# Optimization experiments

Measured on AMD Instinct MI355X. Metric: run time of the kernel, lower is better.

## Reference

```python
import jax, jax.numpy as jnp
import numpy as np

NEG = -9e15


def setup_inputs() -> dict:
    key = jax.random.key(0)
    k1, k2, k3, k4, k5 = jax.random.split(key, 5)
    N, D_IN, D_OUT = 8192, 512, 128
    x = jax.random.normal(k1, (N, D_IN), dtype=jnp.float32)
    adj = jax.random.randint(k2, (N, N), 0, 2, dtype=jnp.int32)
    W_fc = jax.random.normal(k3, (D_IN, D_OUT), dtype=jnp.float32) * (1.0 / np.sqrt(D_IN))
    w_a1 = jax.random.normal(k4, (D_OUT,), dtype=jnp.float32) * (1.0 / np.sqrt(D_OUT))
    w_a2 = jax.random.normal(k5, (D_OUT,), dtype=jnp.float32) * (1.0 / np.sqrt(D_OUT))
    return {"x": x, "adj": adj, "W_fc": W_fc, "w_a1": w_a1, "w_a2": w_a2}


def reference(x, adj, W_fc, w_a1, w_a2):
    # h = fc(x): [N, d_out]
    h = x @ W_fc
    # a1, a2: [N] projections; outer-sum scores a1[i] + a2[j] -> [N, N]
    a1 = h @ w_a1
    a2 = h @ w_a2
    scores = a1[:, None] + a2[None, :]
    # adjacency mask + row softmax
    scores = jnp.where(adj > 0, scores, jnp.float32(NEG))
    attention = jax.nn.softmax(scores, axis=-1)
    # weighted aggregation: [N, N] @ [N, d_out]
    out = attention @ h
    return out  # act == 'None', so no relu
```

## Files before the change

### kernel.cpp

```cpp
#include <hip/hip_runtime.h>
#include <hip/hip_bf16.h>


#define NN 8192
#define DIN 512
#define DOUT 128

typedef __attribute__((ext_vector_type(4))) int   int4v;
typedef __attribute__((ext_vector_type(4))) float f32x4;
typedef __attribute__((ext_vector_type(8))) short bf16x8;

static __device__ __forceinline__ unsigned short f2bf(float f) {
    unsigned u = __float_as_uint(f);
    return (unsigned short)((u + 0x7FFFu + ((u >> 16) & 1u)) >> 16);
}
static __device__ __forceinline__ float bf2f(unsigned short b) {
    return __uint_as_float((unsigned)b << 16);
}
static __device__ __forceinline__ void gload_lds16(const void* g, void* l) {
    __builtin_amdgcn_global_load_lds(
        (const __attribute__((address_space(1))) unsigned*)g,
        (__attribute__((address_space(3))) unsigned*)l, 16, 0, 0);
}
static __device__ __forceinline__ int4v ntld(const int* p) {
    return __builtin_nontemporal_load(reinterpret_cast<const int4v*>(p));
}

__global__ __launch_bounds__(256) void k_cvtW(const float* __restrict__ W,
                                              unsigned short* __restrict__ WT) {
    __shared__ float s[8][128];
    const int t  = threadIdx.x;
    const int k0 = blockIdx.x * 8;
    {
        int idx = t * 4;
        int k = idx >> 7, d = idx & 127;
        float4 v = *reinterpret_cast<const float4*>(&W[(size_t)(k0 + k) * DOUT + d]);
        *reinterpret_cast<float4*>(&s[k][d]) = v;
    }
    __syncthreads();
    const int d  = t & 127;
    const int pl = t >> 7;
    unsigned short o[8];
    #pragma unroll
    for (int kk = 0; kk < 8; ++kk) {
        float f = s[kk][d];
        unsigned short hb = f2bf(f);
        o[kk] = pl ? f2bf(f - bf2f(hb)) : hb;
    }
    *reinterpret_cast<uint4*>(&WT[(size_t)pl * 128 * DIN + (size_t)d * DIN + k0]) =
        *reinterpret_cast<const uint4*>(o);
}

__global__ __launch_bounds__(512, 2) void k_h(const float* __restrict__ x,
                                              const unsigned short* __restrict__ WT,
                                              const float* __restrict__ wa2,
                                              unsigned short* __restrict__ Gt) {
    __shared__ __align__(16) char xls[16384];
    __shared__ float red[8][16];
    __shared__ float es[16];
    const int t = threadIdx.x;
    const int w = t >> 6, l = t & 63;
    const int c = l & 15, g = l >> 4;
    const int j0 = blockIdx.x * 16;

    f32x4 acc = (f32x4)0.f;

    const int srow = t >> 5;
    const int sc4  = t & 31;
    const unsigned wbyte = (unsigned)srow * 256 +
                           (((unsigned)(sc4 * 8)) ^ (((unsigned)(srow & 15)) << 4));
    const float* xp = x + (size_t)(j0 + srow) * DIN + sc4 * 4;

    const unsigned short* bhp = WT + (size_t)(w * 16 + c) * DIN + g * 8;
    const unsigned short* blp = bhp + 128 * DIN;
    const unsigned rswz = ((unsigned)c) << 4;

    float4 xv = *reinterpret_cast<const float4*>(xp);

    for (int kt = 0; kt < 4; ++kt) {
        const int cur = kt & 1;
        char* ph = xls + (cur * 2 + 0) * 4096;
        char* pl_ = xls + (cur * 2 + 1) * 4096;
        {
            float vf[4] = {xv.x, xv.y, xv.z, xv.w};
            unsigned short hb[4], lb[4];
            #pragma unroll
            for (int e2 = 0; e2 < 4; ++e2) {
                hb[e2] = f2bf(vf[e2]);
                lb[e2] = f2bf(vf[e2] - bf2f(hb[e2]));
            }
            uint2 hv = {(unsigned)hb[0] | ((unsigned)hb[1] << 16),
                        (unsigned)hb[2] | ((unsigned)hb[3] << 16)};
            uint2 lv = {(unsigned)lb[0] | ((unsigned)lb[1] << 16),
                        (unsigned)lb[2] | ((unsigned)lb[3] << 16)};
            *reinterpret_cast<uint2*>(ph  + wbyte) = hv;
            *reinterpret_cast<uint2*>(pl_ + wbyte) = lv;
        }
        if (kt < 3) xv = *reinterpret_cast<const float4*>(xp + (kt + 1) * 128);
        __syncthreads();
        #pragma unroll
        for (int ks = 0; ks < 4; ++ks) {
            unsigned ro = ((unsigned)(ks * 64 + g * 16)) ^ rswz;
            bf16x8 ah = *reinterpret_cast<const bf16x8*>(ph  + c * 256 + ro);
            bf16x8 al = *reinterpret_cast<const bf16x8*>(pl_ + c * 256 + ro);
            bf16x8 bh = *reinterpret_cast<const bf16x8*>(bhp + kt * 128 + ks * 32);
            bf16x8 bl = *reinterpret_cast<const bf16x8*>(blp + kt * 128 + ks * 32);
            acc = __builtin_amdgcn_mfma_f32_16x16x32_bf16(ah, bh, acc, 0, 0, 0);
            acc = __builtin_amdgcn_mfma_f32_16x16x32_bf16(ah, bl, acc, 0, 0, 0);
            acc = __builtin_amdgcn_mfma_f32_16x16x32_bf16(al, bh, acc, 0, 0, 0);
        }
        __syncthreads();
    }

    const float wl = wa2[w * 16 + c];
    #pragma unroll
    for (int r = 0; r < 4; ++r) {
        float p = acc[r] * wl;
        p += __shfl_xor(p, 1); p += __shfl_xor(p, 2);
        p += __shfl_xor(p, 4); p += __shfl_xor(p, 8);
        if (c == 0) red[w][g * 4 + r] = p;
    }
    __syncthreads();
    if (t < 16) {
        float s = 0.f;
        #pragma unroll
        for (int ww = 0; ww < 8; ++ww) s += red[ww][t];
        es[t] = expf(s);
    }
    __syncthreads();
    {
        unsigned short b[4];
        #pragma unroll
        for (int r = 0; r < 4; ++r) b[r] = f2bf(acc[r] * es[g * 4 + r]);
        uint2 uv = {(unsigned)b[0] | ((unsigned)b[1] << 16),
                    (unsigned)b[2] | ((unsigned)b[3] << 16)};
        *reinterpret_cast<uint2*>(&Gt[(size_t)(w * 16 + c) * NN + j0 + g * 4]) = uv;
    }
    if (t < 8) {
        unsigned u = (unsigned)f2bf(es[t * 2]) | ((unsigned)f2bf(es[t * 2 + 1]) << 16);
        reinterpret_cast<unsigned*>(&Gt[(size_t)128 * NN + j0])[t] = u;
    }
}

__global__ __launch_bounds__(512, 2) void k_gat(const int* __restrict__ adj,
                                                const unsigned short* __restrict__ Gt,
                                                float* __restrict__ out) {
    __shared__ __align__(16) char lds[86144];
    const int t = threadIdx.x;
    const int w = t >> 6, l = t & 63;
    const int c = l & 15, g = l >> 4;
    const int wm = w >> 2, wc = w & 3;
    const int row0 = blockIdx.x * 32;

    float* denp  = (float*)(lds + 81920);
    float* den_l = (float*)(lds + 86016);

    f32x4 acc0 = (f32x4)0.f, acc1 = (f32x4)0.f;

    const int r0 = t >> 5;
    const int kg = t & 31;
    const int* ap0 = adj + (size_t)(row0 + r0) * NN + kg * 4;
    const int* ap1 = adj + (size_t)(row0 + 16 + r0) * NN + kg * 4;
    const unsigned short* ep = Gt + (size_t)128 * NN + kg * 4;
    const unsigned aswz = ((unsigned)(r0 & 15)) << 4;
    const unsigned aw0  = (unsigned)r0 * 256 + (((unsigned)(kg * 8)) ^ aswz);
    const unsigned aw1  = aw0 + 16 * 256;

    float d0 = 0.f, d1 = 0.f;

    const unsigned arow = (unsigned)(wm * 16 + c);
    const unsigned abase = arow * 256;
    const unsigned afswz = ((unsigned)c) << 4;
    const unsigned br0 = (unsigned)(wc * 32 + c);
    const unsigned br1 = br0 + 16;

    int4v a0 = ntld(ap0), a1 = ntld(ap1);
    uint2 ev = *reinterpret_cast<const uint2*>(ep);
    #pragma unroll
    for (int s = 0; s < 4; ++s) {
        int ii = t + s * 512;
        int rb = ii >> 4, pb = ii & 15;
        int gk = pb ^ (rb & 15);
        gload_lds16(Gt + (size_t)rb * NN + gk * 8, lds + 16384 + ii * 16);
    }
    {
        unsigned u00 = ((unsigned)a0.x | ((unsigned)a0.y << 16)) * 0x3F80u;
        unsigned u01 = ((unsigned)a0.z | ((unsigned)a0.w << 16)) * 0x3F80u;
        unsigned u10 = ((unsigned)a1.x | ((unsigned)a1.y << 16)) * 0x3F80u;
        unsigned u11 = ((unsigned)a1.z | ((unsigned)a1.w << 16)) * 0x3F80u;
        uint2 w0 = {u00, u01}, w1 = {u10, u11};
        *reinterpret_cast<uint2*>(lds + aw0) = w0;
        *reinterpret_cast<uint2*>(lds + aw1) = w1;
        float e0 = bf2f((unsigned short)(ev.x & 0xFFFF)), e1 = bf2f((unsigned short)(ev.x >> 16));
        float e2 = bf2f((unsigned short)(ev.y & 0xFFFF)), e3 = bf2f((unsigned short)(ev.y >> 16));
        d0 += (a0.x ? e0 : 0.f) + (a0.y ? e1 : 0.f) + (a0.z ? e2 : 0.f) + (a0.w ? e3 : 0.f);
        d1 += (a1.x ? e0 : 0.f) + (a1.y ? e1 : 0.f) + (a1.z ? e2 : 0.f) + (a1.w ? e3 : 0.f);
    }
    __syncthreads();

    int cur = 0;
    for (int kt = 0; kt < 64; ++kt) {
        const int nb = cur ^ 1;
        if (kt < 63) {
            const int ko = (kt + 1) * 128;
            a0 = ntld(ap0 + ko);
            a1 = ntld(ap1 + ko);
            ev = *reinterpret_cast<const uint2*>(ep + ko);
            char* Bn = lds + 16384 + nb * 32768;
            #pragma unroll
            for (int s = 0; s < 4; ++s) {
                int ii = t + s * 512;
                int rb = ii >> 4, pb = ii & 15;
                int gk = pb ^ (rb & 15);
                gload_lds16(Gt + (size_t)rb * NN + ko + gk * 8, Bn + ii * 16);
            }
        }
        const char* Ab = lds + cur * 8192;
        const char* Bb = lds + 16384 + cur * 32768;
        #pragma unroll
        for (int ks = 0; ks < 4; ++ks) {
            unsigned ko16 = (unsigned)(ks * 64 + g * 16);
            bf16x8 av = *reinterpret_cast<const bf16x8*>(Ab + abase + (ko16 ^ afswz));
            bf16x8 b0 = *reinterpret_cast<const bf16x8*>(Bb + br0 * 256 + (ko16 ^ (((br0 & 15)) << 4)));
            bf16x8 b1 = *reinterpret_cast<const bf16x8*>(Bb + br1 * 256 + (ko16 ^ (((br1 & 15)) << 4)));
            acc0 = __builtin_amdgcn_mfma_f32_16x16x32_bf16(av, b0, acc0, 0, 0, 0);
            acc1 = __builtin_amdgcn_mfma_f32_16x16x32_bf16(av, b1, acc1, 0, 0, 0);
        }
        if (kt < 63) {
            char* An = lds + nb * 8192;
            unsigned u00 = ((unsigned)a0.x | ((unsigned)a0.y << 16)) * 0x3F80u;
            unsigned u01 = ((unsigned)a0.z | ((unsigned)a0.w << 16)) * 0x3F80u;
            unsigned u10 = ((unsigned)a1.x | ((unsigned)a1.y << 16)) * 0x3F80u;
            unsigned u11 = ((unsigned)a1.z | ((unsigned)a1.w << 16)) * 0x3F80u;
            uint2 w0 = {u00, u01}, w1 = {u10, u11};
            *reinterpret_cast<uint2*>(An + aw0) = w0;
            *reinterpret_cast<uint2*>(An + aw1) = w1;
            float e0 = bf2f((unsigned short)(ev.x & 0xFFFF)), e1 = bf2f((unsigned short)(ev.x >> 16));
            float e2 = bf2f((unsigned short)(ev.y & 0xFFFF)), e3 = bf2f((unsigned short)(ev.y >> 16));
            d0 += (a0.x ? e0 : 0.f) + (a0.y ? e1 : 0.f) + (a0.z ? e2 : 0.f) + (a0.w ? e3 : 0.f);
            d1 += (a1.x ? e0 : 0.f) + (a1.y ? e1 : 0.f) + (a1.z ? e2 : 0.f) + (a1.w ? e3 : 0.f);
        }
        __syncthreads();
        cur ^= 1;
    }

    denp[r0 * 32 + kg] = d0;
    denp[(16 + r0) * 32 + kg] = d1;
    __syncthreads();
    if (t < 32) {
        float s = 0.f;
        #pragma unroll
        for (int q = 0; q < 32; ++q) s += denp[t * 32 + q];
        den_l[t] = s;
    }
    __syncthreads();

    #pragma unroll
    for (int r = 0; r < 4; ++r) {
        float inv = 1.0f / den_l[wm * 16 + g * 4 + r];
        float* orow = out + (size_t)(row0 + wm * 16 + g * 4 + r) * DOUT + wc * 32 + c;
        orow[0]  = acc0[r] * inv;
        orow[16] = acc1[r] * inv;
    }
}

extern "C" void kernel_launch(void* const* d_in, const int* in_sizes, int n_in,
                              void* d_out, int out_size, void* d_ws, size_t ws_size,
                              hipStream_t stream) {
    const float* x   = (const float*)d_in[0];
    const int*   adj = (const int*)d_in[1];
    const float* W   = (const float*)d_in[2];
    const float* wa2 = (const float*)d_in[4];
    float* out = (float*)d_out;

    char* ws = (char*)d_ws;
    unsigned short* WT = (unsigned short*)ws;
    unsigned short* Gt = (unsigned short*)(ws + 262144);

    k_cvtW<<< 64, 256, 0, stream>>>(W, WT);
    k_h   <<<512, 512, 0, stream>>>(x, WT, wa2, Gt);
    k_gat <<<256, 512, 0, stream>>>(adj, Gt, out);
}
```

Measured before the change: 400.5 us.

## Triple-buffer GAT aggregation with partial waitcnt and restructure h projection kernel

The aggregation kernel moves from double to triple buffering of the Gt tiles and adjacency tiles. It uses explicit s_waitcnt vmcnt(7) barriers so loads issued two iterations ahead stay in flight across the barrier, which is meant to hide global load latency on the adj stream that dominates runtime. The cost is more LDS (about 127KB) and the loss of the 2-blocks-per-CU launch bound. The h projection kernel is also rewritten: it uses 256 threads, loads the full x tile at once, and computes two column blocks per wave with register-prefetched W fragments, removing per-k-tile barriers.

```diff
diff --git a/kernel.cpp b/kernel.cpp
--- a/kernel.cpp
+++ b/kernel.cpp
@@ -24,6 +24,9 @@
 }
 static __device__ __forceinline__ int4v ntld(const int* p) {
     return __builtin_nontemporal_load(reinterpret_cast<const int4v*>(p));
+}
+static __device__ __forceinline__ f32x4 ntldf4(const float* p) {
+    return __builtin_nontemporal_load(reinterpret_cast<const f32x4*>(p));
 }
 
 __global__ __launch_bounds__(256) void k_cvtW(const float* __restrict__ W,
@@ -51,90 +54,127 @@
         *reinterpret_cast<const uint4*>(o);
 }
 
-__global__ __launch_bounds__(512, 2) void k_h(const float* __restrict__ x,
-                                              const unsigned short* __restrict__ WT,
-                                              const float* __restrict__ wa2,
-                                              unsigned short* __restrict__ Gt) {
-    __shared__ __align__(16) char xls[16384];
-    __shared__ float red[8][16];
+__global__ __launch_bounds__(256) void k_h(const float* __restrict__ x,
+                                           const unsigned short* __restrict__ WT,
+                                           const float* __restrict__ wa2,
+                                           unsigned short* __restrict__ Gt) {
+    __shared__ __align__(16) char xs[32768];
+    __shared__ float red[4][16];
     __shared__ float es[16];
     const int t = threadIdx.x;
     const int w = t >> 6, l = t & 63;
     const int c = l & 15, g = l >> 4;
     const int j0 = blockIdx.x * 16;
 
-    f32x4 acc = (f32x4)0.f;
-
-    const int srow = t >> 5;
-    const int sc4  = t & 31;
-    const unsigned wbyte = (unsigned)srow * 256 +
-                           (((unsigned)(sc4 * 8)) ^ (((unsigned)(srow & 15)) << 4));
-    const float* xp = x + (size_t)(j0 + srow) * DIN + sc4 * 4;
-
-    const unsigned short* bhp = WT + (size_t)(w * 16 + c) * DIN + g * 8;
-    const unsigned short* blp = bhp + 128 * DIN;
-    const unsigned rswz = ((unsigned)c) << 4;
-
-    float4 xv = *reinterpret_cast<const float4*>(xp);
-
-    for (int kt = 0; kt < 4; ++kt) {
-        const int cur = kt & 1;
-        char* ph = xls + (cur * 2 + 0) * 4096;
-        char* pl_ = xls + (cur * 2 + 1) * 4096;
+    f32x4 xv[8];
+    #pragma unroll
+    for (int s = 0; s < 8; ++s) {
+        int ii = t + s * 256;
+        int r = ii >> 7, k4 = ii & 127;
+        xv[s] = ntldf4(&x[(size_t)(j0 + r) * DIN + k4 * 4]);
+    }
+    #pragma unroll
+    for (int s = 0; s < 8; ++s) {
+        int ii = t + s * 256;
+        int r = ii >> 7, k4 = ii & 127;
+        unsigned byte0 = (unsigned)r * 1024 +
+                         ((((unsigned)(k4 >> 1)) ^ ((unsigned)(r & 15))) << 4) + (k4 & 1) * 8;
+        float vf[4] = {xv[s].x, xv[s].y, xv[s].z, xv[s].w};
+        unsigned short hb[4], lb[4];
+        #pragma unroll
+        for (int e = 0; e < 4; ++e) { hb[e] = f2bf(vf[e]); lb[e] = f2bf(vf[e] - bf2f(hb[e])); }
+        uint2 hv = {(unsigned)hb[0] | ((unsigned)hb[1] << 16),
+                    (unsigned)hb[2] | ((unsigned)hb[3] << 16)};
+        uint2 lv = {(unsigned)lb[0] | ((unsigned)lb[1] << 16),
+                    (unsigned)lb[2] | ((unsigned)lb[3] << 16)};
+        *reinterpret_cast<uint2*>(xs + byte0) = hv;
+        *reinterpret_cast<uint2*>(xs + 16384 + byte0) = lv;
+    }
+    __syncthreads();
+
+    const int wc0 = w * 32;
+    const unsigned short* pB00 = WT + (size_t)(wc0 + c) * DIN + g * 8;
+    const unsigned short* pB01 = pB00 + 16 * DIN;
+    const unsigned short* pB10 = pB00 + 128 * DIN;
+    const unsigned short* pB11 = pB01 + 128 * DIN;
+
+    f32x4 acc0 = (f32x4)0.f, acc1 = (f32x4)0.f;
+    const unsigned arow = (unsigned)c * 1024;
+    const unsigned aswz = (unsigned)(c & 15);
+
+    bf16x8 e00 = *reinterpret_cast<const bf16x8*>(pB00);
+    bf16x8 e01 = *reinterpret_cast<const bf16x8*>(pB01);
+    bf16x8 e10 = *reinterpret_cast<const bf16x8*>(pB10);
+    bf16x8 e11 = *reinterpret_cast<const bf16x8*>(pB11);
+    bf16x8 o00 = *reinterpret_cast<const bf16x8*>(pB00 + 32);
+    bf16x8 o01 = *reinterpret_cast<const bf16x8*>(pB01 + 32);
+    bf16x8 o10 = *reinterpret_cast<const bf16x8*>(pB10 + 32);
+    bf16x8 o11 = *reinterpret_cast<const bf16x8*>(pB11 + 32);
+
+    #pragma unroll
+    for (int ks = 0; ks < 16; ks += 2) {
         {
-            float vf[4] = {xv.x, xv.y, xv.z, xv.w};
-            unsigned short hb[4], lb[4];
-            #pragma unroll
-            for (int e2 = 0; e2 < 4; ++e2) {
-                hb[e2] = f2bf(vf[e2]);
-                lb[e2] = f2bf(vf[e2] - bf2f(hb[e2]));
+            unsigned ab = arow + ((((unsigned)(ks * 4 + g)) ^ aswz) << 4);
+            bf16x8 ahi = *reinterpret_cast<const bf16x8*>(xs + ab);
+            bf16x8 alo = *reinterpret_cast<const bf16x8*>(xs + 16384 + ab);
+            acc0 = __builtin_amdgcn_mfma_f32_16x16x32_bf16(ahi, e00, acc0, 0, 0, 0);
+            acc1 = __builtin_amdgcn_mfma_f32_16x16x32_bf16(ahi, e01, acc1, 0, 0, 0);
+            acc0 = __builtin_amdgcn_mfma_f32_16x16x32_bf16(ahi, e10, acc0, 0, 0, 0);
+            acc1 = __builtin_amdgcn_mfma_f32_16x16x32_bf16(ahi, e11, acc1, 0, 0, 0);
+            acc0 = __builtin_amdgcn_mfma_f32_16x16x32_bf16(alo, e00, acc0, 0, 0, 0);
+            acc1 = __builtin_amdgcn_mfma_f32_16x16x32_bf16(alo, e01, acc1, 0, 0, 0);
+            if (ks + 2 < 16) {
+                e00 = *reinterpret_cast<const bf16x8*>(pB00 + (ks + 2) * 32);
+                e01 = *reinterpret_cast<const bf16x8*>(pB01 + (ks + 2) * 32);
+                e10 = *reinterpret_cast<const bf16x8*>(pB10 + (ks + 2) * 32);
+                e11 = *reinterpret_cast<const bf16x8*>(pB11 + (ks + 2) * 32);
             }
-            uint2 hv = {(unsigned)hb[0] | ((unsigned)hb[1] << 16),
-                        (unsigned)hb[2] | ((unsigned)hb[3] << 16)};
-            uint2 lv = {(unsigned)lb[0] | ((unsigned)lb[1] << 16),
-                        (unsigned)lb[2] | ((unsigned)lb[3] << 16)};
-            *reinterpret_cast<uint2*>(ph  + wbyte) = hv;
-            *reinterpret_cast<uint2*>(pl_ + wbyte) = lv;
         }
-        if (kt < 3) xv = *reinterpret_cast<const float4*>(xp + (kt + 1) * 128);
-        __syncthreads();
-        #pragma unroll
-        for (int ks = 0; ks < 4; ++ks) {
-            unsigned ro = ((unsigned)(ks * 64 + g * 16)) ^ rswz;
-            bf16x8 ah = *reinterpret_cast<const bf16x8*>(ph  + c * 256 + ro);
-            bf16x8 al = *reinterpret_cast<const bf16x8*>(pl_ + c * 256 + ro);
-            bf16x8 bh = *reinterpret_cast<const bf16x8*>(bhp + kt * 128 + ks * 32);
-            bf16x8 bl = *reinterpret_cast<const bf16x8*>(blp + kt * 128 + ks * 32);
-            acc = __builtin_amdgcn_mfma_f32_16x16x32_bf16(ah, bh, acc, 0, 0, 0);
-            acc = __builtin_amdgcn_mfma_f32_16x16x32_bf16(ah, bl, acc, 0, 0, 0);
-            acc = __builtin_amdgcn_mfma_f32_16x16x32_bf16(al, bh, acc, 0, 0, 0);
+        {
+            unsigned ab = arow + ((((unsigned)((ks + 1) * 4 + g)) ^ aswz) << 4);
+            bf16x8 ahi = *reinterpret_cast<const bf16x8*>(xs + ab);
+            bf16x8 alo = *reinterpret_cast<const bf16x8*>(xs + 16384 + ab);
+            acc0 = __builtin_amdgcn_mfma_f32_16x16x32_bf16(ahi, o00, acc0, 0, 0, 0);
+            acc1 = __builtin_amdgcn_mfma_f32_16x16x32_bf16(ahi, o01, acc1, 0, 0, 0);
+            acc0 = __builtin_amdgcn_mfma_f32_16x16x32_bf16(ahi, o10, acc0, 0, 0, 0);
+            acc1 = __builtin_amdgcn_mfma_f32_16x16x32_bf16(ahi, o11, acc1, 0, 0, 0);
+            acc0 = __builtin_amdgcn_mfma_f32_16x16x32_bf16(alo, o00, acc0, 0, 0, 0);
+            acc1 = __builtin_amdgcn_mfma_f32_16x16x32_bf16(alo, o01, acc1, 0, 0, 0);
+            if (ks + 3 < 16) {
+                o00 = *reinterpret_cast<const bf16x8*>(pB00 + (ks + 3) * 32);
+                o01 = *reinterpret_cast<const bf16x8*>(pB01 + (ks + 3) * 32);
+                o10 = *reinterpret_cast<const bf16x8*>(pB10 + (ks + 3) * 32);
+                o11 = *reinterpret_cast<const bf16x8*>(pB11 + (ks + 3) * 32);
+            }
         }
-        __syncthreads();
-    }
-
-    const float wl = wa2[w * 16 + c];
+    }
+
+    const float wl0 = wa2[wc0 + c];
+    const float wl1 = wa2[wc0 + 16 + c];
     #pragma unroll
     for (int r = 0; r < 4; ++r) {
-        float p = acc[r] * wl;
+        float p = acc0[r] * wl0 + acc1[r] * wl1;
         p += __shfl_xor(p, 1); p += __shfl_xor(p, 2);
         p += __shfl_xor(p, 4); p += __shfl_xor(p, 8);
         if (c == 0) red[w][g * 4 + r] = p;
     }
     __syncthreads();
-    if (t < 16) {
-        float s = 0.f;
+    if (t < 16) es[t] = expf(red[0][t] + red[1][t] + red[2][t] + red[3][t]);
+    __syncthreads();
+
+    {
+        unsigned short b0[4], b1[4];
         #pragma unroll
-        for (int ww = 0; ww < 8; ++ww) s += red[ww][t];
-        es[t] = expf(s);
-    }
-    __syncthreads();
-    {
-        unsigned short b[4];
-        #pragma unroll
-        for (int r = 0; r < 4; ++r) b[r] = f2bf(acc[r] * es[g * 4 + r]);
-        uint2 uv = {(unsigned)b[0] | ((unsigned)b[1] << 16),
-                    (unsigned)b[2] | ((unsigned)b[3] << 16)};
-        *reinterpret_cast<uint2*>(&Gt[(size_t)(w * 16 + c) * NN + j0 + g * 4]) = uv;
+        for (int r = 0; r < 4; ++r) {
+            b0[r] = f2bf(acc0[r] * es[g * 4 + r]);
+            b1[r] = f2bf(acc1[r] * es[g * 4 + r]);
+        }
+        uint2 v0 = {(unsigned)b0[0] | ((unsigned)b0[1] << 16),
+                    (unsigned)b0[2] | ((unsigned)b0[3] << 16)};
+        uint2 v1 = {(unsigned)b1[0] | ((unsigned)b1[1] << 16),
+                    (unsigned)b1[2] | ((unsigned)b1[3] << 16)};
+        *reinterpret_cast<uint2*>(&Gt[(size_t)(wc0 + c) * NN + j0 + g * 4]) = v0;
+        *reinterpret_cast<uint2*>(&Gt[(size_t)(wc0 + 16 + c) * NN + j0 + g * 4]) = v1;
     }
     if (t < 8) {
         unsigned u = (unsigned)f2bf(es[t * 2]) | ((unsigned)f2bf(es[t * 2 + 1]) << 16);
@@ -142,107 +182,114 @@
     }
 }
 
-__global__ __launch_bounds__(512, 2) void k_gat(const int* __restrict__ adj,
-                                                const unsigned short* __restrict__ Gt,
-                                                float* __restrict__ out) {
-    __shared__ __align__(16) char lds[86144];
+__global__ __launch_bounds__(512) void k_gat(const int* __restrict__ adj,
+                                             const unsigned short* __restrict__ Gt,
+                                             float* __restrict__ out) {
+    __shared__ __align__(16) char lds[127104];
+    float* denp  = (float*)(lds + 122880);
+    float* den_l = (float*)(lds + 126976);
     const int t = threadIdx.x;
     const int w = t >> 6, l = t & 63;
     const int c = l & 15, g = l >> 4;
     const int wm = w >> 2, wc = w & 3;
     const int row0 = blockIdx.x * 32;
 
-    float* denp  = (float*)(lds + 81920);
-    float* den_l = (float*)(lds + 86016);
-
     f32x4 acc0 = (f32x4)0.f, acc1 = (f32x4)0.f;
+    float d0 = 0.f, d1 = 0.f;
 
     const int r0 = t >> 5;
     const int kg = t & 31;
     const int* ap0 = adj + (size_t)(row0 + r0) * NN + kg * 4;
-    const int* ap1 = adj + (size_t)(row0 + 16 + r0) * NN + kg * 4;
+    const int* ap1 = ap0 + (size_t)16 * NN;
     const unsigned short* ep = Gt + (size_t)128 * NN + kg * 4;
-    const unsigned aswz = ((unsigned)(r0 & 15)) << 4;
-    const unsigned aw0  = (unsigned)r0 * 256 + (((unsigned)(kg * 8)) ^ aswz);
-    const unsigned aw1  = aw0 + 16 * 256;
-
-    float d0 = 0.f, d1 = 0.f;
-
-    const unsigned arow = (unsigned)(wm * 16 + c);
-    const unsigned abase = arow * 256;
+    const unsigned aw0 = (unsigned)r0 * 256 + (((unsigned)(kg * 8)) ^ (((unsigned)(r0 & 15)) << 4));
+    const unsigned aw1 = aw0 + 4096;
+
+    const unsigned abase = ((unsigned)(wm * 16 + c)) * 256;
     const unsigned afswz = ((unsigned)c) << 4;
     const unsigned br0 = (unsigned)(wc * 32 + c);
     const unsigned br1 = br0 + 16;
-
-    int4v a0 = ntld(ap0), a1 = ntld(ap1);
-    uint2 ev = *reinterpret_cast<const uint2*>(ep);
-    #pragma unroll
-    for (int s = 0; s < 4; ++s) {
-        int ii = t + s * 512;
-        int rb = ii >> 4, pb = ii & 15;
-        int gk = pb ^ (rb & 15);
-        gload_lds16(Gt + (size_t)rb * NN + gk * 8, lds + 16384 + ii * 16);
-    }
-    {
-        unsigned u00 = ((unsigned)a0.x | ((unsigned)a0.y << 16)) * 0x3F80u;
-        unsigned u01 = ((unsigned)a0.z | ((unsigned)a0.w << 16)) * 0x3F80u;
-        unsigned u10 = ((unsigned)a1.x | ((unsigned)a1.y << 16)) * 0x3F80u;
-        unsigned u11 = ((unsigned)a1.z | ((unsigned)a1.w << 16)) * 0x3F80u;
-        uint2 w0 = {u00, u01}, w1 = {u10, u11};
-        *reinterpret_cast<uint2*>(lds + aw0) = w0;
-        *reinterpret_cast<uint2*>(lds + aw1) = w1;
-        float e0 = bf2f((unsigned short)(ev.x & 0xFFFF)), e1 = bf2f((unsigned short)(ev.x >> 16));
-        float e2 = bf2f((unsigned short)(ev.y & 0xFFFF)), e3 = bf2f((unsigned short)(ev.y >> 16));
-        d0 += (a0.x ? e0 : 0.f) + (a0.y ? e1 : 0.f) + (a0.z ? e2 : 0.f) + (a0.w ? e3 : 0.f);
-        d1 += (a1.x ? e0 : 0.f) + (a1.y ? e1 : 0.f) + (a1.z ? e2 : 0.f) + (a1.w ? e3 : 0.f);
-    }
-    __syncthreads();
-
-    int cur = 0;
-    for (int kt = 0; kt < 64; ++kt) {
-        const int nb = cur ^ 1;
-        if (kt < 63) {
-            const int ko = (kt + 1) * 128;
-            a0 = ntld(ap0 + ko);
-            a1 = ntld(ap1 + ko);
-            ev = *reinterpret_cast<const uint2*>(ep + ko);
-            char* Bn = lds + 16384 + nb * 32768;
-            #pragma unroll
-            for (int s = 0; s < 4; ++s) {
-                int ii = t + s * 512;
-                int rb = ii >> 4, pb = ii & 15;
-                int gk = pb ^ (rb & 15);
-                gload_lds16(Gt + (size_t)rb * NN + ko + gk * 8, Bn + ii * 16);
-            }
-        }
-        const char* Ab = lds + cur * 8192;
-        const char* Bb = lds + 16384 + cur * 32768;
-        #pragma unroll
-        for (int ks = 0; ks < 4; ++ks) {
-            unsigned ko16 = (unsigned)(ks * 64 + g * 16);
-            bf16x8 av = *reinterpret_cast<const bf16x8*>(Ab + abase + (ko16 ^ afswz));
-            bf16x8 b0 = *reinterpret_cast<const bf16x8*>(Bb + br0 * 256 + (ko16 ^ (((br0 & 15)) << 4)));
-            bf16x8 b1 = *reinterpret_cast<const bf16x8*>(Bb + br1 * 256 + (ko16 ^ (((br1 & 15)) << 4)));
-            acc0 = __builtin_amdgcn_mfma_f32_16x16x32_bf16(av, b0, acc0, 0, 0, 0);
-            acc1 = __builtin_amdgcn_mfma_f32_16x16x32_bf16(av, b1, acc1, 0, 0, 0);
-        }
-        if (kt < 63) {
-            char* An = lds + nb * 8192;
-            unsigned u00 = ((unsigned)a0.x | ((unsigned)a0.y << 16)) * 0x3F80u;
-            unsigned u01 = ((unsigned)a0.z | ((unsigned)a0.w << 16)) * 0x3F80u;
-            unsigned u10 = ((unsigned)a1.x | ((unsigned)a1.y << 16)) * 0x3F80u;
-            unsigned u11 = ((unsigned)a1.z | ((unsigned)a1.w << 16)) * 0x3F80u;
-            uint2 w0 = {u00, u01}, w1 = {u10, u11};
-            *reinterpret_cast<uint2*>(An + aw0) = w0;
-            *reinterpret_cast<uint2*>(An + aw1) = w1;
-            float e0 = bf2f((unsigned short)(ev.x & 0xFFFF)), e1 = bf2f((unsigned short)(ev.x >> 16));
-            float e2 = bf2f((unsigned short)(ev.y & 0xFFFF)), e3 = bf2f((unsigned short)(ev.y >> 16));
-            d0 += (a0.x ? e0 : 0.f) + (a0.y ? e1 : 0.f) + (a0.z ? e2 : 0.f) + (a0.w ? e3 : 0.f);
-            d1 += (a1.x ? e0 : 0.f) + (a1.y ? e1 : 0.f) + (a1.z ? e2 : 0.f) + (a1.w ? e3 : 0.f);
-        }
-        __syncthreads();
-        cur ^= 1;
-    }
+    const unsigned b0base = br0 * 256, b0swz = (br0 & 15) << 4;
+    const unsigned b1base = br1 * 256, b1swz = (br1 & 15) << 4;
+
+#define ISSUE_B(boff, ko) { char* Bn_ = lds + 24576 + (boff); \
+    _Pragma("unroll") for (int s_ = 0; s_ < 4; ++s_) { \
+        int ii_ = t + s_ * 512; int rb_ = ii_ >> 4, pb_ = ii_ & 15; \
+        int gk_ = pb_ ^ (rb_ & 15); \
+        gload_lds16(Gt + (size_t)rb_ * NN + (ko) + gk_ * 8, Bn_ + ii_ * 16); } }
+
+#define LOAD_A(A0, A1, EV, ko) { A0 = ntld(ap0 + (ko)); A1 = ntld(ap1 + (ko)); \
+    EV = *reinterpret_cast<const uint2*>(ep + (ko)); }
+
+#define CONV_A(A0, A1, EV, aoff) { char* An_ = lds + (aoff); \
+    unsigned u00_ = ((unsigned)A0.x | ((unsigned)A0.y << 16)) * 0x3F80u; \
+    unsigned u01_ = ((unsigned)A0.z | ((unsigned)A0.w << 16)) * 0x3F80u; \
+    unsigned u10_ = ((unsigned)A1.x | ((unsigned)A1.y << 16)) * 0x3F80u; \
+    unsigned u11_ = ((unsigned)A1.z | ((unsigned)A1.w << 16)) * 0x3F80u; \
+    uint2 w0_ = {u00_, u01_}, w1_ = {u10_, u11_}; \
+    *reinterpret_cast<uint2*>(An_ + aw0) = w0_; \
+    *reinterpret_cast<uint2*>(An_ + aw1) = w1_; \
+    float e0_ = bf2f((unsigned short)(EV.x & 0xFFFFu)); \
+    float e1_ = bf2f((unsigned short)(EV.x >> 16)); \
+    float e2_ = bf2f((unsigned short)(EV.y & 0xFFFFu)); \
+    float e3_ = bf2f((unsigned short)(EV.y >> 16)); \
+    d0 += (A0.x ? e0_ : 0.f) + (A0.y ? e1_ : 0.f) + (A0.z ? e2_ : 0.f) + (A0.w ? e3_ : 0.f); \
+    d1 += (A1.x ? e0_ : 0.f) + (A1.y ? e1_ : 0.f) + (A1.z ? e2_ : 0.f) + (A1.w ? e3_ : 0.f); }
+
+#define COMPUTE(idx) { const char* Ab_ = lds + (idx) * 8192; \
+    const char* Bb_ = lds + 24576 + (idx) * 32768; \
+    _Pragma("unroll") for (int ks_ = 0; ks_ < 4; ++ks_) { \
+        unsigned ko_ = (unsigned)(ks_ * 64 + g * 16); \
+        bf16x8 av_ = *reinterpret_cast<const bf16x8*>(Ab_ + abase + (ko_ ^ afswz)); \
+        bf16x8 b0_ = *reinterpret_cast<const bf16x8*>(Bb_ + b0base + (ko_ ^ b0swz)); \
+        bf16x8 b1_ = *reinterpret_cast<const bf16x8*>(Bb_ + b1base + (ko_ ^ b1swz)); \
+        acc0 = __builtin_amdgcn_mfma_f32_16x16x32_bf16(av_, b0_, acc0, 0, 0, 0); \
+        acc1 = __builtin_amdgcn_mfma_f32_16x16x32_bf16(av_, b1_, acc1, 0, 0, 0); } }
+
+#define SYNC7() { asm volatile("s_waitcnt vmcnt(7) lgkmcnt(0)" ::: "memory"); \
+    __builtin_amdgcn_sched_barrier(0); __builtin_amdgcn_s_barrier(); \
+    __builtin_amdgcn_sched_barrier(0); }
+#define SYNC0() { asm volatile("s_waitcnt vmcnt(0) lgkmcnt(0)" ::: "memory"); \
+    __builtin_amdgcn_sched_barrier(0); __builtin_amdgcn_s_barrier(); \
+    __builtin_amdgcn_sched_barrier(0); }
+
+    int4v eA0, eA1; uint2 eEv;
+    int4v oA0, oA1; uint2 oEv;
+
+    ISSUE_B(0, 0);
+    LOAD_A(eA0, eA1, eEv, 0);
+    ISSUE_B(32768, 128);
+    LOAD_A(oA0, oA1, oEv, 128);
+    CONV_A(eA0, eA1, eEv, 0);
+    SYNC7();
+
+    int i0 = 0, i1 = 1, i2 = 2;
+    for (int kt = 0; kt < 62; kt += 2) {
+        ISSUE_B(i2 * 32768, (kt + 2) * 128);
+        LOAD_A(eA0, eA1, eEv, (kt + 2) * 128);
+        COMPUTE(i0);
+        CONV_A(oA0, oA1, oEv, i1 * 8192);
+        SYNC7();
+        { int tmp_ = i0; i0 = i1; i1 = i2; i2 = tmp_; }
+        ISSUE_B(i2 * 32768, (kt + 3) * 128);
+        LOAD_A(oA0, oA1, oEv, (kt + 3) * 128);
+        COMPUTE(i0);
+        CONV_A(eA0, eA1, eEv, i1 * 8192);
+        SYNC7();
+        { int tmp_ = i0; i0 = i1; i1 = i2; i2 = tmp_; }
+    }
+    COMPUTE(i0);
+    CONV_A(oA0, oA1, oEv, i1 * 8192);
+    SYNC0();
+    { int tmp_ = i0; i0 = i1; i1 = i2; i2 = tmp_; }
+    COMPUTE(i0);
+
+#undef ISSUE_B
+#undef LOAD_A
+#undef CONV_A
+#undef COMPUTE
+#undef SYNC7
+#undef SYNC0
 
     denp[r0 * 32 + kg] = d0;
     denp[(16 + r0) * 32 + kg] = d1;
@@ -278,6 +325,6 @@
     unsigned short* Gt = (unsigned short*)(ws + 262144);
 
     k_cvtW<<< 64, 256, 0, stream>>>(W, WT);
-    k_h   <<<512, 512, 0, stream>>>(x, WT, wa2, Gt);
+    k_h   <<<512, 256, 0, stream>>>(x, WT, wa2, Gt);
     k_gat <<<256, 512, 0, stream>>>(adj, Gt, out);
 }
```

Result: slower. 410.3 us (+2.4%).
